# Kernel tuning notes

Hardware: AMD Instinct MI355X
Metric: run time of the kernel (lower is better)

Reference implementation:

```python
import jax, jax.numpy as jnp
import numpy as np

N_NODES = 50000
N_EDGES = 800000
IN_DIM_N = 256
IN_DIM_E = 64
OUT_DIM_N = 64
OUT_DIM_E = 64


def setup_inputs() -> dict:
    key = jax.random.key(0)
    ks = jax.random.split(key, 8)
    nfeats = jax.random.normal(ks[0], (N_NODES, IN_DIM_N), dtype=jnp.float32)
    efeats = jax.random.normal(ks[1], (N_EDGES, IN_DIM_E), dtype=jnp.float32)
    src = jax.random.randint(ks[2], (N_EDGES,), 0, N_NODES)
    dst = jax.random.randint(ks[3], (N_EDGES,), 0, N_NODES)
    # xavier-style scaled weights
    W_fc = jax.random.normal(ks[4], (OUT_DIM_N, IN_DIM_N), dtype=jnp.float32) * (2.0 / (OUT_DIM_N + IN_DIM_N)) ** 0.5
    cat_dim = IN_DIM_E + 2 * OUT_DIM_N  # 192
    W_e = jax.random.normal(ks[5], (OUT_DIM_E, cat_dim), dtype=jnp.float32) * (2.0 / (OUT_DIM_E + cat_dim)) ** 0.5
    b_e = jnp.zeros((OUT_DIM_E,), dtype=jnp.float32)
    w_c = jax.random.normal(ks[6], (1, OUT_DIM_E), dtype=jnp.float32) * (2.0 / (1 + OUT_DIM_E)) ** 0.5
    return {"nfeats": nfeats, "efeats": efeats, "src": src, "dst": dst,
            "W_fc": W_fc, "W_e": W_e, "b_e": b_e, "w_c": w_c}


def reference(nfeats, efeats, src, dst, W_fc, W_e, b_e, w_c):
    N = nfeats.shape[0]
    # node projection (no bias)
    z = nfeats @ W_fc.T                                   # [N, out_n]
    # edge attention MLP on [z_src | efeat | z_dst]
    stacked = jnp.concatenate([z[src], efeats, z[dst]], axis=1)  # [E, in_e + 2*out_n]
    feat_e = jax.nn.leaky_relu(stacked @ W_e.T + b_e)     # [E, out_e], slope 0.01 = torch default
    a = (feat_e @ w_c.T)[:, 0]                            # [E]
    # segment softmax over incoming edges of each dst node
    m = jax.ops.segment_max(a, dst, num_segments=N)       # [N] (-inf for empty segs, never gathered)
    ex = jnp.exp(a - m[dst])                              # [E]
    s = jax.ops.segment_sum(ex, dst, num_segments=N)      # [N]
    alpha = ex / s[dst]                                   # [E]
    # weighted scatter-sum aggregate of source z
    h = jax.ops.segment_sum(alpha[:, None] * z[src], dst, num_segments=N)  # [N, out_n]
    return h, feat_e
```

## Files before the change

kernel.cpp:

```cpp
#include <hip/hip_runtime.h>
#include <hip/hip_bf16.h>

#define N_NODES 50000
#define N_EDGES 800000
#define IN_N    256
#define D       64

typedef __attribute__((ext_vector_type(8))) short short8;
typedef __attribute__((ext_vector_type(4))) float f32x4;

__device__ __forceinline__ float bf2f(unsigned short h) {
    union { unsigned int u; float f; } x; x.u = ((unsigned int)h) << 16; return x.f;
}
__device__ __forceinline__ unsigned short f2bf(float f) {
    union { float f; unsigned int u; } x; x.f = f;
    unsigned int r = x.u + 0x7fff + ((x.u >> 16) & 1);
    return (unsigned short)(r >> 16);
}
__device__ __forceinline__ short8 pack8(f32x4 p0, f32x4 p1) {
    short8 r;
    r[0] = (short)f2bf(p0[0]); r[1] = (short)f2bf(p0[1]);
    r[2] = (short)f2bf(p0[2]); r[3] = (short)f2bf(p0[3]);
    r[4] = (short)f2bf(p1[0]); r[5] = (short)f2bf(p1[1]);
    r[6] = (short)f2bf(p1[2]); r[7] = (short)f2bf(p1[3]);
    return r;
}

__global__ void zero_int_kernel(int* __restrict__ p, int n) {
    int i = blockIdx.x * blockDim.x + threadIdx.x;
    int stride = gridDim.x * blockDim.x;
    for (; i < n; i += stride) p[i] = 0;
}

__global__ void count_kernel(const int* __restrict__ dst, int* __restrict__ count) {
    int i = blockIdx.x * blockDim.x + threadIdx.x;
    int stride = gridDim.x * blockDim.x;
    for (; i < N_EDGES / 4; i += stride) {
        int4 d = ((const int4*)dst)[i];
        atomicAdd(&count[d.x], 1);
        atomicAdd(&count[d.y], 1);
        atomicAdd(&count[d.z], 1);
        atomicAdd(&count[d.w], 1);
    }
}

__global__ __launch_bounds__(1024) void scan_kernel(const int* __restrict__ count,
                                                    int* __restrict__ offsets,
                                                    int* __restrict__ cursor) {
    __shared__ int part[1024];
    const int t = threadIdx.x;
    const int C = (N_NODES + 1023) / 1024;
    const int base = t * C;
    int s = 0;
    for (int i = 0; i < C; ++i) {
        int idx = base + i;
        if (idx < N_NODES) s += count[idx];
    }
    part[t] = s;
    __syncthreads();
    for (int st = 1; st < 1024; st <<= 1) {
        int v = (t >= st) ? part[t - st] : 0;
        __syncthreads();
        part[t] += v;
        __syncthreads();
    }
    int run = part[t] - s;
    for (int i = 0; i < C; ++i) {
        int idx = base + i;
        if (idx < N_NODES) {
            offsets[idx] = run;
            cursor[idx]  = run;
            run += count[idx];
        }
    }
    if (t == 1023) offsets[N_NODES] = part[1023];
}

__global__ __launch_bounds__(256) void proj_kernel(
    const float* __restrict__ nf, const float* __restrict__ W_fc,
    unsigned short* __restrict__ z_bf)
{
    __shared__ unsigned short wl[64 * 264];
    for (int i = threadIdx.x; i < 64 * 256; i += 256)
        wl[(i >> 8) * 264 + (i & 255)] = f2bf(W_fc[i]);
    __syncthreads();
    const int lanelo = threadIdx.x & 15, quad = (threadIdx.x >> 4) & 3;
    const int wflat = blockIdx.x * 4 + (threadIdx.x >> 6);
    const int nw = gridDim.x * 4;
    const f32x4 z4 = {0.f, 0.f, 0.f, 0.f};
    for (int g = wflat; g < N_NODES / 16; g += nw) {
        const int n0 = g * 16;
        f32x4 acc[4] = {z4, z4, z4, z4};
        const float* arow = nf + (size_t)(n0 + lanelo) * IN_N;
        #pragma unroll
        for (int h = 0; h < 8; ++h) {
            const float* ap = arow + h * 32 + quad * 8;
            f32x4 p0 = *(const f32x4*)ap;
            f32x4 p1 = *(const f32x4*)(ap + 4);
            short8 a = pack8(p0, p1);
            #pragma unroll
            for (int t = 0; t < 4; ++t) {
                short8 b = *(const short8*)&wl[(t * 16 + lanelo) * 264 + h * 32 + quad * 8];
                acc[t] = __builtin_amdgcn_mfma_f32_16x16x32_bf16(a, b, acc[t], 0, 0, 0);
            }
        }
        #pragma unroll
        for (int t = 0; t < 4; ++t)
            #pragma unroll
            for (int r = 0; r < 4; ++r)
                z_bf[(size_t)(n0 + quad * 4 + r) * D + t * 16 + lanelo] = f2bf(acc[t][r]);
    }
}

__global__ __launch_bounds__(256) void uv_kernel(
    const unsigned short* __restrict__ z_bf, const float* __restrict__ W_e,
    const float* __restrict__ b_e,
    unsigned short* __restrict__ u_bf, unsigned short* __restrict__ v_bf)
{
    __shared__ unsigned short wl[128 * 72];
    for (int i = threadIdx.x; i < 128 * 64; i += 256) {
        int row = i >> 6, col = i & 63;
        float val = (row < 64) ? W_e[(size_t)row * 192 + col]
                               : W_e[(size_t)(row - 64) * 192 + 128 + col];
        wl[row * 72 + col] = f2bf(val);
    }
    __syncthreads();
    const int lanelo = threadIdx.x & 15, quad = (threadIdx.x >> 4) & 3;
    float bias[4];
    #pragma unroll
    for (int t = 0; t < 4; ++t) bias[t] = b_e[t * 16 + lanelo];
    const int wflat = blockIdx.x * 4 + (threadIdx.x >> 6);
    const int nw = gridDim.x * 4;
    const f32x4 z4 = {0.f, 0.f, 0.f, 0.f};
    for (int g = wflat; g < N_NODES / 16; g += nw) {
        const int n0 = g * 16;
        f32x4 acc[8] = {z4, z4, z4, z4, z4, z4, z4, z4};
        #pragma unroll
        for (int h = 0; h < 2; ++h) {
            short8 a = *(const short8*)(z_bf + (size_t)(n0 + lanelo) * D + h * 32 + quad * 8);
            #pragma unroll
            for (int t = 0; t < 8; ++t) {
                short8 b = *(const short8*)&wl[(t * 16 + lanelo) * 72 + h * 32 + quad * 8];
                acc[t] = __builtin_amdgcn_mfma_f32_16x16x32_bf16(a, b, acc[t], 0, 0, 0);
            }
        }
        #pragma unroll
        for (int t = 0; t < 4; ++t)
            #pragma unroll
            for (int r = 0; r < 4; ++r)
                u_bf[(size_t)(n0 + quad * 4 + r) * D + t * 16 + lanelo] = f2bf(acc[t][r] + bias[t]);
        #pragma unroll
        for (int t = 4; t < 8; ++t)
            #pragma unroll
            for (int r = 0; r < 4; ++r)
                v_bf[(size_t)(n0 + quad * 4 + r) * D + (t - 4) * 16 + lanelo] = f2bf(acc[t][r]);
    }
}

__global__ __launch_bounds__(256) void edge_kernel(
    const float* __restrict__ efeats,
    const int* __restrict__ src, const int* __restrict__ dst,
    const float* __restrict__ W_e, const float* __restrict__ w_c,
    const unsigned short* __restrict__ u_bf, const unsigned short* __restrict__ v_bf,
    int* __restrict__ cursor, unsigned long long* __restrict__ csr,
    float* __restrict__ feat_out)
{
    const int lanelo = threadIdx.x & 15, quad = (threadIdx.x >> 4) & 3;
    short8 b2[4][2];
    #pragma unroll
    for (int t = 0; t < 4; ++t)
        #pragma unroll
        for (int h = 0; h < 2; ++h)
            #pragma unroll
            for (int j = 0; j < 8; ++j)
                b2[t][h][j] = (short)f2bf(W_e[(size_t)(t * 16 + lanelo) * 192 + 64 + h * 32 + quad * 8 + j]);
    float wcv[4];
    #pragma unroll
    for (int t = 0; t < 4; ++t) wcv[t] = w_c[t * 16 + lanelo];

    const int wflat = blockIdx.x * 4 + (threadIdx.x >> 6);
    const int nw = gridDim.x * 4;
    const f32x4 z4 = {0.f, 0.f, 0.f, 0.f};
    for (int g = wflat; g < N_EDGES / 16; g += nw) {
        const int e0 = g * 16;
        f32x4 acc[4] = {z4, z4, z4, z4};
        const float* ar = efeats + (size_t)(e0 + lanelo) * D;
        #pragma unroll
        for (int h = 0; h < 2; ++h) {
            f32x4 p0 = *(const f32x4*)(ar + h * 32 + quad * 8);
            f32x4 p1 = *(const f32x4*)(ar + h * 32 + quad * 8 + 4);
            short8 a = pack8(p0, p1);
            #pragma unroll
            for (int t = 0; t < 4; ++t)
                acc[t] = __builtin_amdgcn_mfma_f32_16x16x32_bf16(a, b2[t][h], acc[t], 0, 0, 0);
        }
        int sn[4], dn[4];
        #pragma unroll
        for (int r = 0; r < 4; ++r) {
            sn[r] = src[e0 + quad * 4 + r];
            dn[r] = dst[e0 + quad * 4 + r];
        }
        float part[4];
        #pragma unroll
        for (int r = 0; r < 4; ++r) {
            float p = 0.f;
            #pragma unroll
            for (int t = 0; t < 4; ++t) {
                float f = acc[t][r]
                        + bf2f(u_bf[(size_t)sn[r] * D + t * 16 + lanelo])
                        + bf2f(v_bf[(size_t)dn[r] * D + t * 16 + lanelo]);
                f = f > 0.f ? f : 0.01f * f;
                feat_out[(size_t)(e0 + quad * 4 + r) * D + t * 16 + lanelo] = f;
                p += f * wcv[t];
            }
            part[r] = p;
        }
        #pragma unroll
        for (int st = 1; st < 16; st <<= 1) {
            #pragma unroll
            for (int r = 0; r < 4; ++r) part[r] += __shfl_xor(part[r], st, 64);
        }
        #pragma unroll
        for (int r = 0; r < 4; ++r) {
            float ex = __expf(part[r]);
            if (lanelo == 0) {
                int pos = atomicAdd(&cursor[dn[r]], 1);
                csr[pos] = ((unsigned long long)__float_as_uint(ex) << 32)
                         | (unsigned long long)(unsigned int)sn[r];
            }
        }
    }
}

__global__ __launch_bounds__(256) void agg_kernel(
    const unsigned long long* __restrict__ csr,
    const int* __restrict__ offsets,
    const unsigned short* __restrict__ z_bf,
    float* __restrict__ h)
{
    const int lane = threadIdx.x & 63;
    const int wid = (blockIdx.x * blockDim.x + threadIdx.x) >> 6;
    const int nw = (gridDim.x * blockDim.x) >> 6;
    for (int n = wid; n < N_NODES; n += nw) {
        const int off = offsets[n];
        const int end = offsets[n + 1];
        float acc = 0.f, ssum = 0.f;
        int e = off;
        for (; e + 1 < end; e += 2) {
            unsigned long long p0 = csr[e];
            unsigned long long p1 = csr[e + 1];
            float x0 = __uint_as_float((unsigned int)(p0 >> 32));
            float x1 = __uint_as_float((unsigned int)(p1 >> 32));
            int s0 = (int)(p0 & 0xffffffffu);
            int s1 = (int)(p1 & 0xffffffffu);
            float z0 = bf2f(z_bf[(size_t)s0 * D + lane]);
            float z1 = bf2f(z_bf[(size_t)s1 * D + lane]);
            acc += x0 * z0;
            acc += x1 * z1;
            ssum += x0 + x1;
        }
        if (e < end) {
            unsigned long long p0 = csr[e];
            float x0 = __uint_as_float((unsigned int)(p0 >> 32));
            int s0 = (int)(p0 & 0xffffffffu);
            acc += x0 * bf2f(z_bf[(size_t)s0 * D + lane]);
            ssum += x0;
        }
        h[(size_t)n * D + lane] = ssum > 0.f ? acc / ssum : 0.f;
    }
}

extern "C" void kernel_launch(void* const* d_in, const int* in_sizes, int n_in,
                              void* d_out, int out_size, void* d_ws, size_t ws_size,
                              hipStream_t stream)
{
    const float* nfeats = (const float*)d_in[0];
    const float* efeats = (const float*)d_in[1];
    const int* src = (const int*)d_in[2];
    const int* dst = (const int*)d_in[3];
    const float* W_fc = (const float*)d_in[4];
    const float* W_e  = (const float*)d_in[5];
    const float* b_e  = (const float*)d_in[6];
    const float* w_c  = (const float*)d_in[7];

    unsigned short* z_bf = (unsigned short*)d_ws;
    unsigned short* u_bf = z_bf + (size_t)N_NODES * D;
    unsigned short* v_bf = u_bf + (size_t)N_NODES * D;
    unsigned long long* csr = (unsigned long long*)(v_bf + (size_t)N_NODES * D);
    int* count   = (int*)(csr + (size_t)N_EDGES);
    int* offsets = count + N_NODES;
    int* cursor  = offsets + N_NODES + 1;

    float* h_out = (float*)d_out;
    float* f_out = h_out + (size_t)N_NODES * D;

    zero_int_kernel<<<64, 256, 0, stream>>>(count, N_NODES);
    count_kernel<<<512, 256, 0, stream>>>(dst, count);
    scan_kernel<<<1, 1024, 0, stream>>>(count, offsets, cursor);
    proj_kernel<<<782, 256, 0, stream>>>(nfeats, W_fc, z_bf);
    uv_kernel<<<782, 256, 0, stream>>>(z_bf, W_e, b_e, u_bf, v_bf);
    edge_kernel<<<2048, 256, 0, stream>>>(efeats, src, dst, W_e, w_c, u_bf, v_bf,
                                          cursor, csr, f_out);
    agg_kernel<<<2048, 256, 0, stream>>>(csr, offsets, z_bf, h_out);
}
```

Before: 709.3 us.

## Fold edge weights into node projection, fuse node kernels, shuffle-batch aggregation

A prep kernel precomputes the products W_e_src·W_fc and W_e_dst·W_fc in bf16, so one node kernel produces z, u and v straight from nfeats. This removes the separate uv pass and its reread of z. Efeats loads and feat_out stores become nontemporal, and the aggregation loads 64 CSR entries per wave at once and broadcasts them with shuffles, unrolled by four. The zero kernel is replaced by hipMemsetAsync. The node kernel now runs three times the MFMAs and reads its weights from global memory instead of LDS, and folding the weights changes the bf16 rounding.

```diff
diff --git a/kernel.cpp b/kernel.cpp
--- a/kernel.cpp
+++ b/kernel.cpp
@@ -24,12 +24,6 @@
     r[4] = (short)f2bf(p1[0]); r[5] = (short)f2bf(p1[1]);
     r[6] = (short)f2bf(p1[2]); r[7] = (short)f2bf(p1[3]);
     return r;
-}
-
-__global__ void zero_int_kernel(int* __restrict__ p, int n) {
-    int i = blockIdx.x * blockDim.x + threadIdx.x;
-    int stride = gridDim.x * blockDim.x;
-    for (; i < n; i += stride) p[i] = 0;
 }
 
 __global__ void count_kernel(const int* __restrict__ dst, int* __restrict__ count) {
@@ -76,55 +70,34 @@
     if (t == 1023) offsets[N_NODES] = part[1023];
 }
 
-__global__ __launch_bounds__(256) void proj_kernel(
-    const float* __restrict__ nf, const float* __restrict__ W_fc,
-    unsigned short* __restrict__ z_bf)
-{
-    __shared__ unsigned short wl[64 * 264];
-    for (int i = threadIdx.x; i < 64 * 256; i += 256)
-        wl[(i >> 8) * 264 + (i & 255)] = f2bf(W_fc[i]);
-    __syncthreads();
-    const int lanelo = threadIdx.x & 15, quad = (threadIdx.x >> 4) & 3;
-    const int wflat = blockIdx.x * 4 + (threadIdx.x >> 6);
-    const int nw = gridDim.x * 4;
-    const f32x4 z4 = {0.f, 0.f, 0.f, 0.f};
-    for (int g = wflat; g < N_NODES / 16; g += nw) {
-        const int n0 = g * 16;
-        f32x4 acc[4] = {z4, z4, z4, z4};
-        const float* arow = nf + (size_t)(n0 + lanelo) * IN_N;
-        #pragma unroll
-        for (int h = 0; h < 8; ++h) {
-            const float* ap = arow + h * 32 + quad * 8;
-            f32x4 p0 = *(const f32x4*)ap;
-            f32x4 p1 = *(const f32x4*)(ap + 4);
-            short8 a = pack8(p0, p1);
-            #pragma unroll
-            for (int t = 0; t < 4; ++t) {
-                short8 b = *(const short8*)&wl[(t * 16 + lanelo) * 264 + h * 32 + quad * 8];
-                acc[t] = __builtin_amdgcn_mfma_f32_16x16x32_bf16(a, b, acc[t], 0, 0, 0);
-            }
-        }
-        #pragma unroll
-        for (int t = 0; t < 4; ++t)
-            #pragma unroll
-            for (int r = 0; r < 4; ++r)
-                z_bf[(size_t)(n0 + quad * 4 + r) * D + t * 16 + lanelo] = f2bf(acc[t][r]);
-    }
-}
-
-__global__ __launch_bounds__(256) void uv_kernel(
-    const unsigned short* __restrict__ z_bf, const float* __restrict__ W_e,
-    const float* __restrict__ b_e,
-    unsigned short* __restrict__ u_bf, unsigned short* __restrict__ v_bf)
-{
-    __shared__ unsigned short wl[128 * 72];
-    for (int i = threadIdx.x; i < 128 * 64; i += 256) {
-        int row = i >> 6, col = i & 63;
-        float val = (row < 64) ? W_e[(size_t)row * 192 + col]
-                               : W_e[(size_t)(row - 64) * 192 + 128 + col];
-        wl[row * 72 + col] = f2bf(val);
-    }
-    __syncthreads();
+__global__ void prep_kernel(const float* __restrict__ W_fc, const float* __restrict__ W_e,
+                            unsigned short* __restrict__ Wz,
+                            unsigned short* __restrict__ Wu,
+                            unsigned short* __restrict__ Wv)
+{
+    int flat = blockIdx.x * blockDim.x + threadIdx.x;
+    if (flat >= 3 * 64 * 256) return;
+    int mat = flat >> 14;
+    int idx = flat & 16383;
+    if (mat == 0) {
+        Wz[idx] = f2bf(W_fc[idx]);
+        return;
+    }
+    int o = idx >> 8, i = idx & 255;
+    const float* wrow = W_e + (size_t)o * 192 + (mat == 2 ? 128 : 0);
+    float s = 0.f;
+    #pragma unroll 8
+    for (int j = 0; j < 64; ++j) s += wrow[j] * W_fc[(size_t)j * 256 + i];
+    (mat == 1 ? Wu : Wv)[idx] = f2bf(s);
+}
+
+__global__ __launch_bounds__(256) void node_kernel(
+    const float* __restrict__ nf,
+    const unsigned short* __restrict__ Wz, const unsigned short* __restrict__ Wu,
+    const unsigned short* __restrict__ Wv, const float* __restrict__ b_e,
+    unsigned short* __restrict__ z_bf, unsigned short* __restrict__ u_bf,
+    unsigned short* __restrict__ v_bf)
+{
     const int lanelo = threadIdx.x & 15, quad = (threadIdx.x >> 4) & 3;
     float bias[4];
     #pragma unroll
@@ -134,26 +107,34 @@
     const f32x4 z4 = {0.f, 0.f, 0.f, 0.f};
     for (int g = wflat; g < N_NODES / 16; g += nw) {
         const int n0 = g * 16;
-        f32x4 acc[8] = {z4, z4, z4, z4, z4, z4, z4, z4};
-        #pragma unroll
-        for (int h = 0; h < 2; ++h) {
-            short8 a = *(const short8*)(z_bf + (size_t)(n0 + lanelo) * D + h * 32 + quad * 8);
-            #pragma unroll
-            for (int t = 0; t < 8; ++t) {
-                short8 b = *(const short8*)&wl[(t * 16 + lanelo) * 72 + h * 32 + quad * 8];
-                acc[t] = __builtin_amdgcn_mfma_f32_16x16x32_bf16(a, b, acc[t], 0, 0, 0);
+        f32x4 az[4] = {z4, z4, z4, z4};
+        f32x4 au[4] = {z4, z4, z4, z4};
+        f32x4 av[4] = {z4, z4, z4, z4};
+        const float* arow = nf + (size_t)(n0 + lanelo) * IN_N;
+        #pragma unroll
+        for (int h = 0; h < 8; ++h) {
+            const float* ap = arow + h * 32 + quad * 8;
+            f32x4 p0 = *(const f32x4*)ap;
+            f32x4 p1 = *(const f32x4*)(ap + 4);
+            short8 a = pack8(p0, p1);
+            const int bo = h * 32 + quad * 8;
+            #pragma unroll
+            for (int t = 0; t < 4; ++t) {
+                const size_t rb = (size_t)(t * 16 + lanelo) * 256 + bo;
+                az[t] = __builtin_amdgcn_mfma_f32_16x16x32_bf16(a, *(const short8*)&Wz[rb], az[t], 0, 0, 0);
+                au[t] = __builtin_amdgcn_mfma_f32_16x16x32_bf16(a, *(const short8*)&Wu[rb], au[t], 0, 0, 0);
+                av[t] = __builtin_amdgcn_mfma_f32_16x16x32_bf16(a, *(const short8*)&Wv[rb], av[t], 0, 0, 0);
             }
         }
         #pragma unroll
         for (int t = 0; t < 4; ++t)
             #pragma unroll
-            for (int r = 0; r < 4; ++r)
-                u_bf[(size_t)(n0 + quad * 4 + r) * D + t * 16 + lanelo] = f2bf(acc[t][r] + bias[t]);
-        #pragma unroll
-        for (int t = 4; t < 8; ++t)
-            #pragma unroll
-            for (int r = 0; r < 4; ++r)
-                v_bf[(size_t)(n0 + quad * 4 + r) * D + (t - 4) * 16 + lanelo] = f2bf(acc[t][r]);
+            for (int r = 0; r < 4; ++r) {
+                const size_t row = (size_t)(n0 + quad * 4 + r) * D + t * 16 + lanelo;
+                z_bf[row] = f2bf(az[t][r]);
+                u_bf[row] = f2bf(au[t][r] + bias[t]);
+                v_bf[row] = f2bf(av[t][r]);
+            }
     }
 }
 
@@ -187,8 +168,8 @@
         const float* ar = efeats + (size_t)(e0 + lanelo) * D;
         #pragma unroll
         for (int h = 0; h < 2; ++h) {
-            f32x4 p0 = *(const f32x4*)(ar + h * 32 + quad * 8);
-            f32x4 p1 = *(const f32x4*)(ar + h * 32 + quad * 8 + 4);
+            f32x4 p0 = __builtin_nontemporal_load((const f32x4*)(ar + h * 32 + quad * 8));
+            f32x4 p1 = __builtin_nontemporal_load((const f32x4*)(ar + h * 32 + quad * 8 + 4));
             short8 a = pack8(p0, p1);
             #pragma unroll
             for (int t = 0; t < 4; ++t)
@@ -210,7 +191,7 @@
                         + bf2f(u_bf[(size_t)sn[r] * D + t * 16 + lanelo])
                         + bf2f(v_bf[(size_t)dn[r] * D + t * 16 + lanelo]);
                 f = f > 0.f ? f : 0.01f * f;
-                feat_out[(size_t)(e0 + quad * 4 + r) * D + t * 16 + lanelo] = f;
+                __builtin_nontemporal_store(f, &feat_out[(size_t)(e0 + quad * 4 + r) * D + t * 16 + lanelo]);
                 p += f * wcv[t];
             }
             part[r] = p;
@@ -243,28 +224,36 @@
     const int nw = (gridDim.x * blockDim.x) >> 6;
     for (int n = wid; n < N_NODES; n += nw) {
         const int off = offsets[n];
-        const int end = offsets[n + 1];
+        const int d = offsets[n + 1] - off;
         float acc = 0.f, ssum = 0.f;
-        int e = off;
-        for (; e + 1 < end; e += 2) {
-            unsigned long long p0 = csr[e];
-            unsigned long long p1 = csr[e + 1];
-            float x0 = __uint_as_float((unsigned int)(p0 >> 32));
-            float x1 = __uint_as_float((unsigned int)(p1 >> 32));
-            int s0 = (int)(p0 & 0xffffffffu);
-            int s1 = (int)(p1 & 0xffffffffu);
-            float z0 = bf2f(z_bf[(size_t)s0 * D + lane]);
-            float z1 = bf2f(z_bf[(size_t)s1 * D + lane]);
-            acc += x0 * z0;
-            acc += x1 * z1;
-            ssum += x0 + x1;
-        }
-        if (e < end) {
-            unsigned long long p0 = csr[e];
-            float x0 = __uint_as_float((unsigned int)(p0 >> 32));
-            int s0 = (int)(p0 & 0xffffffffu);
-            acc += x0 * bf2f(z_bf[(size_t)s0 * D + lane]);
-            ssum += x0;
+        for (int base = 0; base < d; base += 64) {
+            const int cnt = min(d - base, 64);
+            unsigned long long pk = csr[off + base + min(lane, cnt - 1)];
+            unsigned int hi = (unsigned int)(pk >> 32);
+            unsigned int lo = (unsigned int)pk;
+            int j = 0;
+            for (; j + 4 <= cnt; j += 4) {
+                float x0 = __uint_as_float(__shfl((int)hi, j,     64));
+                float x1 = __uint_as_float(__shfl((int)hi, j + 1, 64));
+                float x2 = __uint_as_float(__shfl((int)hi, j + 2, 64));
+                float x3 = __uint_as_float(__shfl((int)hi, j + 3, 64));
+                int s0 = __shfl((int)lo, j,     64);
+                int s1 = __shfl((int)lo, j + 1, 64);
+                int s2 = __shfl((int)lo, j + 2, 64);
+                int s3 = __shfl((int)lo, j + 3, 64);
+                float z0 = bf2f(z_bf[(size_t)s0 * D + lane]);
+                float z1 = bf2f(z_bf[(size_t)s1 * D + lane]);
+                float z2 = bf2f(z_bf[(size_t)s2 * D + lane]);
+                float z3 = bf2f(z_bf[(size_t)s3 * D + lane]);
+                acc += x0 * z0; acc += x1 * z1; acc += x2 * z2; acc += x3 * z3;
+                ssum += (x0 + x1) + (x2 + x3);
+            }
+            for (; j < cnt; ++j) {
+                float xj = __uint_as_float(__shfl((int)hi, j, 64));
+                int sj = __shfl((int)lo, j, 64);
+                acc += xj * bf2f(z_bf[(size_t)sj * D + lane]);
+                ssum += xj;
+            }
         }
         h[(size_t)n * D + lane] = ssum > 0.f ? acc / ssum : 0.f;
     }
@@ -287,18 +276,21 @@
     unsigned short* u_bf = z_bf + (size_t)N_NODES * D;
     unsigned short* v_bf = u_bf + (size_t)N_NODES * D;
     unsigned long long* csr = (unsigned long long*)(v_bf + (size_t)N_NODES * D);
-    int* count   = (int*)(csr + (size_t)N_EDGES);
+    unsigned short* Wz = (unsigned short*)(csr + (size_t)N_EDGES);
+    unsigned short* Wu = Wz + 64 * 256;
+    unsigned short* Wv = Wu + 64 * 256;
+    int* count   = (int*)(Wv + 64 * 256);
     int* offsets = count + N_NODES;
     int* cursor  = offsets + N_NODES + 1;
 
     float* h_out = (float*)d_out;
     float* f_out = h_out + (size_t)N_NODES * D;
 
-    zero_int_kernel<<<64, 256, 0, stream>>>(count, N_NODES);
+    hipMemsetAsync(count, 0, N_NODES * sizeof(int), stream);
     count_kernel<<<512, 256, 0, stream>>>(dst, count);
     scan_kernel<<<1, 1024, 0, stream>>>(count, offsets, cursor);
-    proj_kernel<<<782, 256, 0, stream>>>(nfeats, W_fc, z_bf);
-    uv_kernel<<<782, 256, 0, stream>>>(z_bf, W_e, b_e, u_bf, v_bf);
+    prep_kernel<<<192, 256, 0, stream>>>(W_fc, W_e, Wz, Wu, Wv);
+    node_kernel<<<782, 256, 0, stream>>>(nfeats, Wz, Wu, Wv, b_e, z_bf, u_bf, v_bf);
     edge_kernel<<<2048, 256, 0, stream>>>(efeats, src, dst, W_e, w_c, u_bf, v_bf,
                                           cursor, csr, f_out);
     agg_kernel<<<2048, 256, 0, stream>>>(csr, offsets, z_bf, h_out);
```

Result: no change. 722.3 us (+1.8%).
